# Kernel optimization log

Measured on AMD Instinct MI355X. Metric: run time of the kernel, lower is better.

## Reference

```python
import jax, jax.numpy as jnp
import numpy as np

K = 7          # kernel_size
PAD = K // 2   # padding = 3
G = 16         # groups = channels // group_channels = 256 // 16
GC = 16        # group_channels
EPS = 1e-5     # BatchNorm eps


def setup_inputs() -> dict:
    key = jax.random.key(0)
    ks = jax.random.split(key, 8)
    B, C, H, W = 4, 256, 56, 56
    Cr = C // 4  # reduction_ratio = 4
    x = jax.random.normal(ks[0], (B, C, H, W), dtype=jnp.float32)
    W_reduce = jax.random.normal(ks[1], (Cr, C), dtype=jnp.float32) * 0.05
    b_reduce = jax.random.normal(ks[2], (Cr,), dtype=jnp.float32) * 0.01
    bn_gamma = jnp.ones((Cr,), dtype=jnp.float32)
    bn_beta = jnp.zeros((Cr,), dtype=jnp.float32)
    bn_mean = jax.random.normal(ks[3], (Cr,), dtype=jnp.float32) * 0.01
    bn_var = jax.random.uniform(ks[4], (Cr,), dtype=jnp.float32, minval=0.5, maxval=1.5)
    W_span = jax.random.normal(ks[5], (K * K * G, Cr), dtype=jnp.float32) * 0.05
    b_span = jax.random.normal(ks[6], (K * K * G,), dtype=jnp.float32) * 0.01
    return {
        "x": x,
        "W_reduce": W_reduce, "b_reduce": b_reduce,
        "bn_gamma": bn_gamma, "bn_beta": bn_beta,
        "bn_mean": bn_mean, "bn_var": bn_var,
        "W_span": W_span, "b_span": b_span,
    }


def _involution(x, W_reduce, b_reduce, bn_gamma, bn_beta, bn_mean, bn_var, W_span, b_span):
    B, C, H, W = x.shape
    # --- kernel generation path (stride=1 -> initial_mapping is Identity) ---
    # 1x1 conv reduce: [B, Cr, H, W]
    xr = jnp.einsum('oc,bchw->bohw', W_reduce, x) + b_reduce[None, :, None, None]
    # BatchNorm (eval mode, running stats) + ReLU
    inv_std = jax.lax.rsqrt(bn_var + EPS)
    xr = (xr - bn_mean[None, :, None, None]) * (bn_gamma * inv_std)[None, :, None, None] \
         + bn_beta[None, :, None, None]
    xr = jax.nn.relu(xr)
    # 1x1 conv span: [B, K*K*G, H, W] -> [B, G, K^2, H*W]
    kern = jnp.einsum('oc,bchw->bohw', W_span, xr) + b_span[None, :, None, None]
    kern = kern.reshape(B, G, K * K, H * W)
    # --- unfold: sliding K x K windows, torch ordering (c, kh, kw) ---
    xp = jnp.pad(x, ((0, 0), (0, 0), (PAD, PAD), (PAD, PAD)))
    # [B, C, K^2, H, W]; fixed 49-iteration loop over kernel offsets
    patches = jnp.stack(
        [xp[:, :, i:i + H, j:j + W] for i in range(K) for j in range(K)], axis=2)
    patches = patches.reshape(B, G, GC, K * K, H * W)
    # multiply dynamic kernels (broadcast over group_channels) and reduce over K^2
    out = jnp.einsum('bgkl,bgckl->bgcl', kern, patches)
    return out.reshape(B, C, H, W)


def reference(x, W_reduce, b_reduce, bn_gamma, bn_beta, bn_mean, bn_var, W_span, b_span):
    return _involution(x, W_reduce, b_reduce, bn_gamma, bn_beta,
                       bn_mean, bn_var, W_span, b_span)
```

## Files before the change

### kernel.cpp

```cpp
#include <hip/hip_runtime.h>
#include <hip/hip_bf16.h>

#define HW    3136
#define C_IN  256
#define G_    16
#define GC_   16
#define IMGH  56
#define IMGW  56
#define EPSV  1e-5f

typedef __bf16 bf16x8 __attribute__((ext_vector_type(8)));
typedef float  f32x4  __attribute__((ext_vector_type(4)));

static __device__ __forceinline__ unsigned short f2bf(float f) {
    union { float f; unsigned u; } v; v.f = f;
    unsigned r = (v.u + 0x7FFFu + ((v.u >> 16) & 1u)) >> 16;
    return (unsigned short)r;
}

static __device__ __forceinline__ bf16x8 pack8(const float* p) {
    union { unsigned short s[8]; bf16x8 v; } u;
#pragma unroll
    for (int j = 0; j < 8; ++j) u.s[j] = f2bf(p[j]);
    return u.v;
}

__global__ __launch_bounds__(256) void k_reduce(
    const float* __restrict__ x,  const float* __restrict__ Wr,
    const float* __restrict__ br, const float* __restrict__ gamma,
    const float* __restrict__ beta, const float* __restrict__ mean,
    const float* __restrict__ var, unsigned short* __restrict__ xrT)
{
    int t = threadIdx.x, wv = t >> 6, lane = t & 63;
    int ln = lane & 15, quad = lane >> 4;
    int p = blockIdx.x * 64 + wv * 16 + ln;
    int b = p / HW, l = p - b * HW;
    const float* xb = x + (size_t)b * C_IN * HW + l;

    f32x4 acc[4];
#pragma unroll
    for (int mt = 0; mt < 4; ++mt) acc[mt] = (f32x4){0.f, 0.f, 0.f, 0.f};

#pragma unroll
    for (int ks = 0; ks < 8; ++ks) {
        int c0 = ks * 32 + quad * 8;
        float xv[8];
#pragma unroll
        for (int j = 0; j < 8; ++j) xv[j] = xb[(size_t)(c0 + j) * HW];
        union { unsigned short s[8]; bf16x8 v; } bfx;
#pragma unroll
        for (int j = 0; j < 8; ++j) bfx.s[j] = f2bf(xv[j]);
#pragma unroll
        for (int mt = 0; mt < 4; ++mt) {
            bf16x8 af = pack8(Wr + (size_t)(mt * 16 + ln) * C_IN + c0);
            acc[mt] = __builtin_amdgcn_mfma_f32_16x16x32_bf16(af, bfx.v, acc[mt], 0, 0, 0);
        }
    }
#pragma unroll
    for (int mt = 0; mt < 4; ++mt) {
        union { unsigned short s[4]; uint2 v; } pk;
#pragma unroll
        for (int r = 0; r < 4; ++r) {
            int o = mt * 16 + quad * 4 + r;
            float s  = gamma[o] * rsqrtf(var[o] + EPSV);
            float vv = (acc[mt][r] + br[o] - mean[o]) * s + beta[o];
            pk.s[r] = f2bf(fmaxf(vv, 0.f));
        }
        *(uint2*)(xrT + (size_t)p * 64 + mt * 16 + quad * 4) = pk.v;
    }
}

#define CSTRIDE 500
#define KSTR    124

__global__ __launch_bounds__(512) void k_invol(
    const float* __restrict__ x, const unsigned short* __restrict__ xrT,
    const float* __restrict__ Wspan, const float* __restrict__ bspan,
    float* __restrict__ out)
{
    __shared__ float s_x[GC_ * CSTRIDE];
    __shared__ float s_kern[49 * KSTR];

    int t = threadIdx.x;
    int bid = blockIdx.x;
    int xcd = bid & 7, jj = bid >> 3;
    int g = jj & 15, rpb = jj >> 4;
    int idx = xcd * 14 + rpb;
    int b = idx / 28, rp = idx - b * 28;
    int h0 = rp * 2;

    const float* xg = x + (size_t)(b * C_IN + g * GC_) * HW;
    float xreg[16];
#pragma unroll
    for (int it = 0; it < 16; ++it) {
        int i = t + 512 * it;
        int c = i / 496;
        int rem = i - c * 496;
        int rr = rem / 62, col = rem - rr * 62;
        int hr = h0 + rr - 3, wc = col - 3;
        float v = 0.f;
        if (c < GC_ && hr >= 0 && hr < IMGH && wc >= 0 && wc < IMGW)
            v = xg[(size_t)c * HW + hr * IMGW + wc];
        xreg[it] = v;
    }

    {
        int wv = t >> 6, lane = t & 63;
        int ln = lane & 15, quad = lane >> 4;
        int mt = wv & 3, nh = wv >> 2;
        int m0 = mt * 16;
        int ko_a = m0 + ln; if (ko_a > 48) ko_a = 48;
        const float* wrow = Wspan + (size_t)(g * 49 + ko_a) * 64;
        int pixbase = b * HW + h0 * IMGW;

        f32x4 acc[4];
#pragma unroll
        for (int nt = 0; nt < 4; ++nt) acc[nt] = (f32x4){0.f, 0.f, 0.f, 0.f};

#pragma unroll
        for (int ks = 0; ks < 2; ++ks) {
            int c0 = ks * 32 + quad * 8;
            bf16x8 af = pack8(wrow + c0);
#pragma unroll
            for (int nt = 0; nt < 4; ++nt) {
                int pp = nh * 64 + nt * 16 + ln;
                if (pp > 111) pp = 111;
                bf16x8 bb = *(const bf16x8*)(xrT + (size_t)(pixbase + pp) * 64 + c0);
                acc[nt] = __builtin_amdgcn_mfma_f32_16x16x32_bf16(af, bb, acc[nt], 0, 0, 0);
            }
        }
#pragma unroll
        for (int r = 0; r < 4; ++r) {
            int ko = m0 + quad * 4 + r;
            float bias = bspan[g * 49 + (ko < 49 ? ko : 48)];
#pragma unroll
            for (int nt = 0; nt < 4; ++nt) {
                int pp = nh * 64 + nt * 16 + ln;
                if (ko < 49 && pp < 112) {
                    int prow = pp / 56, pw = pp - prow * 56;
                    s_kern[ko * KSTR + prow * 60 + pw] = acc[nt][r] + bias;
                }
            }
        }
    }

#pragma unroll
    for (int it = 0; it < 16; ++it) {
        int i = t + 512 * it;
        int c = i / 496;
        int rem = i - c * 496;
        int rr = rem / 62, col = rem - rr * 62;
        if (c < GC_) s_x[c * CSTRIDE + rr * 62 + col] = xreg[it];
    }
    __syncthreads();

    if (t < 448) {
        int row = t / 224, rem = t - row * 224;
        int wq = rem % 14, c = rem / 14;
        int w0 = wq * 4;
        const float* sx = s_x + c * CSTRIDE + row * 62;
        const float* sk = s_kern + row * 60 + w0;
        float a0 = 0.f, a1 = 0.f, a2 = 0.f, a3 = 0.f;
#pragma unroll
        for (int r = 0; r < 7; ++r) {
            float xv[10];
#pragma unroll
            for (int q = 0; q < 10; ++q) xv[q] = sx[r * 62 + w0 + q];
#pragma unroll
            for (int dw = 0; dw < 7; ++dw) {
                float4 kv = *(const float4*)(sk + (r * 7 + dw) * KSTR);
                a0 += kv.x * xv[dw];
                a1 += kv.y * xv[dw + 1];
                a2 += kv.z * xv[dw + 2];
                a3 += kv.w * xv[dw + 3];
            }
        }
        *(float4*)(out + (size_t)(b * C_IN + g * GC_ + c) * HW
                       + (h0 + row) * IMGW + w0) = make_float4(a0, a1, a2, a3);
    }
}

extern "C" void kernel_launch(void* const* d_in, const int* in_sizes, int n_in,
                              void* d_out, int out_size, void* d_ws, size_t ws_size,
                              hipStream_t stream)
{
    const float* x   = (const float*)d_in[0];
    const float* Wr  = (const float*)d_in[1];
    const float* br  = (const float*)d_in[2];
    const float* gm  = (const float*)d_in[3];
    const float* bt  = (const float*)d_in[4];
    const float* mn  = (const float*)d_in[5];
    const float* vr  = (const float*)d_in[6];
    const float* Ws  = (const float*)d_in[7];
    const float* bs  = (const float*)d_in[8];
    float* out = (float*)d_out;

    unsigned short* xrT = (unsigned short*)d_ws;

    k_reduce<<<dim3(196), 256, 0, stream>>>(x, Wr, br, gm, bt, mn, vr, xrT);
    k_invol<<<dim3(1792), 512, 0, stream>>>(x, xrT, Ws, bs, out);
}
```

Before: 124.6 us.

## Pre-pad input and pre-convert weights to bf16; read x from global in involution

Adds a padding kernel that writes a zero-padded copy of x so the involution kernel can read rows straight from global/L2 without bounds checks, and drops the shared-memory staging of x. Adds a weight-conversion kernel so both reduce and span GEMMs load bf16 weights directly. The reduce kernel is re-split to one 16-output tile per wave across 4x more blocks, and the involution inner loop computes a 2-channel by 2-pixel tile that reuses kernel values across channels. The cost is two extra launches and a full extra write and read of a padded copy of x (about 16 MB).

After: 142.3 us. +14.2%, slower.

```diff
diff --git a/kernel.cpp b/kernel.cpp
--- a/kernel.cpp
+++ b/kernel.cpp
@@ -9,6 +9,10 @@
 #define IMGW  56
 #define EPSV  1e-5f
 
+#define PROWS 62
+#define PRSTR 64
+#define KSTR  118
+
 typedef __bf16 bf16x8 __attribute__((ext_vector_type(8)));
 typedef float  f32x4  __attribute__((ext_vector_type(4)));
 
@@ -18,29 +22,58 @@
     return (unsigned short)r;
 }
 
-static __device__ __forceinline__ bf16x8 pack8(const float* p) {
-    union { unsigned short s[8]; bf16x8 v; } u;
-#pragma unroll
-    for (int j = 0; j < 8; ++j) u.s[j] = f2bf(p[j]);
-    return u.v;
+__global__ __launch_bounds__(256) void k_pad(
+    const float* __restrict__ x, float* __restrict__ xpad)
+{
+    int F0 = blockIdx.x * 1024 + threadIdx.x;
+#pragma unroll
+    for (int it = 0; it < 4; ++it) {
+        int F   = F0 + it * 256;
+        int bc  = F / 992;
+        int rem = F - bc * 992;
+        int row = rem >> 4, col4 = (rem & 15) << 2;
+        int hr  = row - 3;
+        const float* xs = x + (size_t)bc * HW + hr * IMGW;
+        float4 v;
+        float* vp = (float*)&v;
+#pragma unroll
+        for (int j = 0; j < 4; ++j) {
+            int wc = col4 + j - 3;
+            vp[j] = (hr >= 0 && hr < IMGH && wc >= 0 && wc < IMGW) ? xs[wc] : 0.f;
+        }
+        *(float4*)(xpad + (size_t)bc * (PROWS * PRSTR) + row * PRSTR + col4) = v;
+    }
+}
+
+__global__ __launch_bounds__(256) void k_wcvt(
+    const float* __restrict__ Wr, const float* __restrict__ Wspan,
+    unsigned short* __restrict__ Wbf, unsigned short* __restrict__ Wsbf)
+{
+    int i4 = (blockIdx.x * 256 + threadIdx.x) * 4;
+    if (i4 < 16384) {
+#pragma unroll
+        for (int j = 0; j < 4; ++j) Wbf[i4 + j] = f2bf(Wr[i4 + j]);
+    } else {
+        int j0 = i4 - 16384;
+#pragma unroll
+        for (int j = 0; j < 4; ++j) Wsbf[j0 + j] = f2bf(Wspan[j0 + j]);
+    }
 }
 
 __global__ __launch_bounds__(256) void k_reduce(
-    const float* __restrict__ x,  const float* __restrict__ Wr,
+    const float* __restrict__ x,  const unsigned short* __restrict__ Wbf,
     const float* __restrict__ br, const float* __restrict__ gamma,
     const float* __restrict__ beta, const float* __restrict__ mean,
     const float* __restrict__ var, unsigned short* __restrict__ xrT)
 {
     int t = threadIdx.x, wv = t >> 6, lane = t & 63;
     int ln = lane & 15, quad = lane >> 4;
-    int p = blockIdx.x * 64 + wv * 16 + ln;
-    int b = p / HW, l = p - b * HW;
+    int p = blockIdx.x * 16 + ln;
+    int b = blockIdx.x / 196;
+    int l = p - b * HW;
     const float* xb = x + (size_t)b * C_IN * HW + l;
 
-    f32x4 acc[4];
-#pragma unroll
-    for (int mt = 0; mt < 4; ++mt) acc[mt] = (f32x4){0.f, 0.f, 0.f, 0.f};
-
+    f32x4 acc = (f32x4){0.f, 0.f, 0.f, 0.f};
 #pragma unroll
     for (int ks = 0; ks < 8; ++ks) {
         int c0 = ks * 32 + quad * 8;
@@ -50,35 +83,25 @@
         union { unsigned short s[8]; bf16x8 v; } bfx;
 #pragma unroll
         for (int j = 0; j < 8; ++j) bfx.s[j] = f2bf(xv[j]);
-#pragma unroll
-        for (int mt = 0; mt < 4; ++mt) {
-            bf16x8 af = pack8(Wr + (size_t)(mt * 16 + ln) * C_IN + c0);
-            acc[mt] = __builtin_amdgcn_mfma_f32_16x16x32_bf16(af, bfx.v, acc[mt], 0, 0, 0);
-        }
-    }
-#pragma unroll
-    for (int mt = 0; mt < 4; ++mt) {
-        union { unsigned short s[4]; uint2 v; } pk;
-#pragma unroll
-        for (int r = 0; r < 4; ++r) {
-            int o = mt * 16 + quad * 4 + r;
-            float s  = gamma[o] * rsqrtf(var[o] + EPSV);
-            float vv = (acc[mt][r] + br[o] - mean[o]) * s + beta[o];
-            pk.s[r] = f2bf(fmaxf(vv, 0.f));
-        }
-        *(uint2*)(xrT + (size_t)p * 64 + mt * 16 + quad * 4) = pk.v;
-    }
-}
-
-#define CSTRIDE 500
-#define KSTR    124
+        bf16x8 af = *(const bf16x8*)(Wbf + (size_t)(wv * 16 + ln) * C_IN + c0);
+        acc = __builtin_amdgcn_mfma_f32_16x16x32_bf16(af, bfx.v, acc, 0, 0, 0);
+    }
+    union { unsigned short s[4]; uint2 v; } pk;
+#pragma unroll
+    for (int r = 0; r < 4; ++r) {
+        int o = wv * 16 + quad * 4 + r;
+        float s  = gamma[o] * rsqrtf(var[o] + EPSV);
+        float vv = (acc[r] + br[o] - mean[o]) * s + beta[o];
+        pk.s[r] = f2bf(fmaxf(vv, 0.f));
+    }
+    *(uint2*)(xrT + (size_t)p * 64 + wv * 16 + quad * 4) = pk.v;
+}
 
 __global__ __launch_bounds__(512) void k_invol(
-    const float* __restrict__ x, const unsigned short* __restrict__ xrT,
-    const float* __restrict__ Wspan, const float* __restrict__ bspan,
+    const float* __restrict__ xpad, const unsigned short* __restrict__ xrT,
+    const unsigned short* __restrict__ Wsbf, const float* __restrict__ bspan,
     float* __restrict__ out)
 {
-    __shared__ float s_x[GC_ * CSTRIDE];
     __shared__ float s_kern[49 * KSTR];
 
     int t = threadIdx.x;
@@ -89,28 +112,13 @@
     int b = idx / 28, rp = idx - b * 28;
     int h0 = rp * 2;
 
-    const float* xg = x + (size_t)(b * C_IN + g * GC_) * HW;
-    float xreg[16];
-#pragma unroll
-    for (int it = 0; it < 16; ++it) {
-        int i = t + 512 * it;
-        int c = i / 496;
-        int rem = i - c * 496;
-        int rr = rem / 62, col = rem - rr * 62;
-        int hr = h0 + rr - 3, wc = col - 3;
-        float v = 0.f;
-        if (c < GC_ && hr >= 0 && hr < IMGH && wc >= 0 && wc < IMGW)
-            v = xg[(size_t)c * HW + hr * IMGW + wc];
-        xreg[it] = v;
-    }
-
     {
         int wv = t >> 6, lane = t & 63;
         int ln = lane & 15, quad = lane >> 4;
         int mt = wv & 3, nh = wv >> 2;
         int m0 = mt * 16;
         int ko_a = m0 + ln; if (ko_a > 48) ko_a = 48;
-        const float* wrow = Wspan + (size_t)(g * 49 + ko_a) * 64;
+        const unsigned short* wrow = Wsbf + (size_t)(g * 49 + ko_a) * 64;
         int pixbase = b * HW + h0 * IMGW;
 
         f32x4 acc[4];
@@ -120,7 +128,7 @@
 #pragma unroll
         for (int ks = 0; ks < 2; ++ks) {
             int c0 = ks * 32 + quad * 8;
-            bf16x8 af = pack8(wrow + c0);
+            bf16x8 af = *(const bf16x8*)(wrow + c0);
 #pragma unroll
             for (int nt = 0; nt < 4; ++nt) {
                 int pp = nh * 64 + nt * 16 + ln;
@@ -138,45 +146,50 @@
                 int pp = nh * 64 + nt * 16 + ln;
                 if (ko < 49 && pp < 112) {
                     int prow = pp / 56, pw = pp - prow * 56;
-                    s_kern[ko * KSTR + prow * 60 + pw] = acc[nt][r] + bias;
+                    s_kern[ko * KSTR + prow * 58 + pw] = acc[nt][r] + bias;
                 }
             }
         }
-    }
-
-#pragma unroll
-    for (int it = 0; it < 16; ++it) {
-        int i = t + 512 * it;
-        int c = i / 496;
-        int rem = i - c * 496;
-        int rr = rem / 62, col = rem - rr * 62;
-        if (c < GC_) s_x[c * CSTRIDE + rr * 62 + col] = xreg[it];
     }
     __syncthreads();
 
     if (t < 448) {
         int row = t / 224, rem = t - row * 224;
-        int wq = rem % 14, c = rem / 14;
-        int w0 = wq * 4;
-        const float* sx = s_x + c * CSTRIDE + row * 62;
-        const float* sk = s_kern + row * 60 + w0;
-        float a0 = 0.f, a1 = 0.f, a2 = 0.f, a3 = 0.f;
+        int cp = rem / 28, wp = rem - cp * 28;
+        int w0 = wp * 2;
+        int c0 = cp * 2;
+
+        const float* xr0 = xpad + ((size_t)(b * C_IN + g * GC_ + c0) * PROWS
+                                   + (h0 + row)) * PRSTR + w0;
+        const float* xr1 = xr0 + PROWS * PRSTR;
+        const float* skb = s_kern + row * 58 + w0;
+
+        float a00 = 0.f, a01 = 0.f, a10 = 0.f, a11 = 0.f;
 #pragma unroll
         for (int r = 0; r < 7; ++r) {
-            float xv[10];
-#pragma unroll
-            for (int q = 0; q < 10; ++q) xv[q] = sx[r * 62 + w0 + q];
+            float2 kv[7];
+#pragma unroll
+            for (int dw = 0; dw < 7; ++dw)
+                kv[dw] = *(const float2*)(skb + (r * 7 + dw) * KSTR);
+            float xa[8], xc[8];
+#pragma unroll
+            for (int j = 0; j < 4; ++j) {
+                float2 u = *(const float2*)(xr0 + r * PRSTR + 2 * j);
+                xa[2 * j] = u.x; xa[2 * j + 1] = u.y;
+                float2 w = *(const float2*)(xr1 + r * PRSTR + 2 * j);
+                xc[2 * j] = w.x; xc[2 * j + 1] = w.y;
+            }
 #pragma unroll
             for (int dw = 0; dw < 7; ++dw) {
-                float4 kv = *(const float4*)(sk + (r * 7 + dw) * KSTR);
-                a0 += kv.x * xv[dw];
-                a1 += kv.y * xv[dw + 1];
-                a2 += kv.z * xv[dw + 2];
-                a3 += kv.w * xv[dw + 3];
-            }
-        }
-        *(float4*)(out + (size_t)(b * C_IN + g * GC_ + c) * HW
-                       + (h0 + row) * IMGW + w0) = make_float4(a0, a1, a2, a3);
+                a00 += kv[dw].x * xa[dw];
+                a01 += kv[dw].y * xa[dw + 1];
+                a10 += kv[dw].x * xc[dw];
+                a11 += kv[dw].y * xc[dw + 1];
+            }
+        }
+        float* ob = out + (size_t)(b * C_IN + g * GC_ + c0) * HW + (h0 + row) * IMGW + w0;
+        *(float2*)ob = make_float2(a00, a01);
+        *(float2*)(ob + HW) = make_float2(a10, a11);
     }
 }
 
@@ -195,8 +208,14 @@
     const float* bs  = (const float*)d_in[8];
     float* out = (float*)d_out;
 
-    unsigned short* xrT = (unsigned short*)d_ws;
-
-    k_reduce<<<dim3(196), 256, 0, stream>>>(x, Wr, br, gm, bt, mn, vr, xrT);
-    k_invol<<<dim3(1792), 512, 0, stream>>>(x, xrT, Ws, bs, out);
-}
+    char* ws = (char*)d_ws;
+    unsigned short* xrT  = (unsigned short*)ws;
+    float*          xpad = (float*)(ws + 1605632);
+    unsigned short* Wbf  = (unsigned short*)(ws + 17858560);
+    unsigned short* Wsbf = (unsigned short*)(ws + 17891328);
+
+    k_wcvt  <<<dim3(65),   256, 0, stream>>>(Wr, Ws, Wbf, Wsbf);
+    k_pad   <<<dim3(992),  256, 0, stream>>>(x, xpad);
+    k_reduce<<<dim3(784),  256, 0, stream>>>(x, Wbf, br, gm, bt, mn, vr, xrT);
+    k_invol <<<dim3(1792), 512, 0, stream>>>(xpad, xrT, Wsbf, bs, out);
+}
```
